# Optimization experiments

Measured on AMD Instinct MI355X. Metric: run time of the kernel, lower is better.

The kernel has to match this reference:

```python
import jax, jax.numpy as jnp
import numpy as np
import math

DIM = 1024

def setup_inputs() -> dict:
    key = jax.random.key(0)
    ks = jax.random.split(key, 5)
    X = jax.random.normal(ks[0], (4, 2048, DIM), dtype=jnp.float32)
    # Linear params (stored as [in, out] so y = x @ W + b)
    W_in = jax.random.normal(ks[1], (DIM, 3 * DIM), dtype=jnp.float32) / math.sqrt(DIM)
    b_in = jnp.zeros((3 * DIM,), dtype=jnp.float32)
    W_out = jax.random.normal(ks[2], (DIM, DIM), dtype=jnp.float32) / math.sqrt(DIM)
    b_out = jnp.zeros((DIM,), dtype=jnp.float32)
    return {"X": X, "W_in": W_in, "b_in": b_in, "W_out": W_out, "b_out": b_out}

def reference(X, W_in, b_in, W_out, b_out):
    dim = X.shape[-1]
    QKV = X @ W_in + b_in                       # [B, S, 3*dim]
    Q, K, V = jnp.split(QKV, 3, axis=-1)        # each [B, S, dim]
    scores = jnp.einsum('bqd,bkd->bqk', Q, K) / math.sqrt(dim)  # [B, S, S]
    attn = jax.nn.softmax(scores, axis=-1)
    out = jnp.einsum('bqk,bkd->bqd', attn, V)   # [B, S, dim]
    return out @ W_out + b_out
```

## Files before the change

### kernel.cpp

```cpp
#include <hip/hip_runtime.h>
#include <hip/hip_bf16.h>
#include <math.h>

typedef __attribute__((ext_vector_type(8))) __bf16 bf16x8;
typedef __attribute__((ext_vector_type(4))) float f32x4;
typedef __attribute__((ext_vector_type(4))) unsigned int u32x4;

#define DIM 1024
#define SEQ 2048
#define BATCH 4
#define ROWS (BATCH*SEQ)

#define BAR() do { asm volatile("" ::: "memory"); __builtin_amdgcn_s_barrier(); asm volatile("" ::: "memory"); } while(0)
#define WAITV(n) asm volatile("s_waitcnt vmcnt(" #n ")" ::: "memory")
#define WAITL0() asm volatile("s_waitcnt lgkmcnt(0)" ::: "memory")
#define SCHED0() __builtin_amdgcn_sched_barrier(0)
#define PRIO(x) __builtin_amdgcn_s_setprio(x)

#define DSR(d, a, off) do { u32x4 _t; \
  asm volatile("ds_read_b128 %0, %1 offset:" #off : "=v"(_t) : "v"(a)); \
  (d) = __builtin_bit_cast(bf16x8, _t); } while(0)

__device__ __forceinline__ unsigned short f2bf(float f) {
  unsigned int u = __float_as_uint(f);
  u += 0x7FFF + ((u >> 16) & 1);
  return (unsigned short)(u >> 16);
}
__device__ __forceinline__ unsigned short to_bf_bits(float v) { return f2bf(v); }
__device__ __forceinline__ unsigned short to_bf_bits(unsigned short v) { return v; }

__device__ __forceinline__ void gload_lds16(const void* g, void* lds) {
  __builtin_amdgcn_global_load_lds((__attribute__((address_space(1))) void*)g,
                                   (__attribute__((address_space(3))) void*)lds,
                                   16, 0, 0);
}

__global__ __launch_bounds__(256)
void conv_f32_bf16(const float* __restrict__ src, unsigned short* __restrict__ dst, int n8) {
  int i = blockIdx.x * blockDim.x + threadIdx.x;
  if (i >= n8) return;
  const float4* s = reinterpret_cast<const float4*>(src) + (size_t)i * 2;
  float4 a = s[0], b = s[1];
  union { unsigned short h[8]; uint4 v; } p;
  p.h[0]=f2bf(a.x); p.h[1]=f2bf(a.y); p.h[2]=f2bf(a.z); p.h[3]=f2bf(a.w);
  p.h[4]=f2bf(b.x); p.h[5]=f2bf(b.y); p.h[6]=f2bf(b.z); p.h[7]=f2bf(b.w);
  reinterpret_cast<uint4*>(dst)[i] = p.v;
}

template<typename Tin>
__global__ __launch_bounds__(1024)
void transpose_conv(const Tin* __restrict__ src, int ldsrc, size_t sstride,
                    unsigned short* __restrict__ dst, int lddst, size_t dstride) {
  __shared__ unsigned short tile[32][33];
  const Tin* s = src + (size_t)blockIdx.z * sstride;
  unsigned short* d = dst + (size_t)blockIdx.z * dstride;
  int tx = threadIdx.x, ty = threadIdx.y;
  int r = blockIdx.y * 32 + ty, c = blockIdx.x * 32 + tx;
  tile[ty][tx] = to_bf_bits(s[(size_t)r * ldsrc + c]);
  __syncthreads();
  d[(size_t)(blockIdx.x * 32 + ty) * lddst + blockIdx.y * 32 + tx] = tile[tx][ty];
}

#define EPI_QKV 0
#define EPI_F32 1
#define EPI_BF16 2
#define EPI_BIAS_F32 3

template<int BN, int EPI>
__global__ __launch_bounds__(512, 2)
void gemm8(const unsigned short* __restrict__ A, int lda, size_t sA,
           const unsigned short* __restrict__ B, int ldb, size_t sB,
           void* __restrict__ C, int ldc, size_t sC,
           const float* __restrict__ bias, int K) {
  constexpr int NREP = BN / 64;
  constexpr int NW = 16 * NREP;
  __shared__ unsigned short As[2 * 256 * 64];
  __shared__ unsigned short Bs[2 * BN * 64];

  const int tid = threadIdx.x;
  const int lane = tid & 63, wave = tid >> 6;
  const int wm = wave >> 2, wn = wave & 3;
  const int fr = lane & 15, fk = lane >> 4;
  const int tileM = blockIdx.y * 256, tileN = blockIdx.x * BN;
  const unsigned short* Ab = A + (size_t)blockIdx.z * sA;
  const unsigned short* Bb = B + (size_t)blockIdx.z * sB;

  const int srow = tid >> 3;
  const int sg = (tid & 7) ^ (srow & 7);

  auto stageA = [&](int buf, int half, int k0) {
#pragma unroll
    for (int q = 0; q < 2; ++q) {
      int rl = half * 128 + q * 64 + srow;
      gload_lds16(Ab + (size_t)(tileM + rl) * lda + k0 + sg * 8,
                  &As[buf * (256 * 64) + rl * 64 + (tid & 7) * 8]);
    }
  };
  auto stageB = [&](int buf, int half, int k0) {
#pragma unroll
    for (int q = 0; q < 2; ++q) {
      int rl = half * 128 + q * 64 + srow;
      gload_lds16(Bb + (size_t)(tileN + rl) * ldb + k0 + sg * 8,
                  &Bs[buf * (BN * 64) + rl * 64 + (tid & 7) * 8]);
    }
  };

  f32x4 acc[8][NREP];
#pragma unroll
  for (int m = 0; m < 8; ++m)
#pragma unroll
    for (int n = 0; n < NREP; ++n) acc[m][n] = (f32x4){0.f, 0.f, 0.f, 0.f};

  const int NS = K >> 6;
  const unsigned asb = (unsigned)(size_t)(__attribute__((address_space(3))) unsigned short*)As;
  const unsigned bsb = (unsigned)(size_t)(__attribute__((address_space(3))) unsigned short*)Bs;
  const unsigned aoff = (unsigned)((wm * 128 + fr) * 128 + ((fk ^ (fr & 7)) << 4));
  const unsigned boff = (unsigned)((wn * NW + fr) * 128 + ((fk ^ (fr & 7)) << 4));

  if constexpr (BN == 256) {
    stageB(0, 0, 0); stageB(0, 1, 0); stageA(0, 0, 0); stageA(0, 1, 0);
    if (NS > 1) { stageB(1, 0, 64); stageB(1, 1, 64); WAITV(4); } else { WAITV(0); }
  } else {
    stageB(0, 0, 0); stageA(0, 0, 0); stageA(0, 1, 0);
    if (NS > 1) { stageB(1, 0, 64); WAITV(2); } else { WAITV(0); }
  }
  BAR();

  bf16x8 afLo[4][2], afHi[4][2], bgA[2][2], bgB[2][2];

  for (int t = 0; t < NS; ++t) {
    const int cb = t & 1, nb = cb ^ 1;
    const unsigned aA0 = asb + (unsigned)cb * 32768u + aoff, aA1 = aA0 ^ 64u;
    const unsigned bB0 = bsb + (unsigned)cb * (unsigned)(BN * 128) + boff, bB1 = bB0 ^ 64u;
    const int k1 = (t + 1) << 6, k2 = (t + 2) << 6;

    if constexpr (BN == 256) {
      DSR(afLo[0][0], aA0, 0); DSR(afLo[1][0], aA0, 2048); DSR(afLo[2][0], aA0, 4096); DSR(afLo[3][0], aA0, 6144);
      DSR(afLo[0][1], aA1, 0); DSR(afLo[1][1], aA1, 2048); DSR(afLo[2][1], aA1, 4096); DSR(afLo[3][1], aA1, 6144);
      DSR(bgA[0][0], bB0, 0); DSR(bgA[1][0], bB0, 2048);
      DSR(bgA[0][1], bB1, 0); DSR(bgA[1][1], bB1, 2048);
      if (t + 1 < NS) stageA(nb, 0, k1);
      BAR(); WAITL0(); SCHED0();
      PRIO(1);
#pragma unroll
      for (int kk = 0; kk < 2; ++kk)
#pragma unroll
        for (int m = 0; m < 4; ++m)
#pragma unroll
          for (int n = 0; n < 2; ++n)
            acc[m][n] = __builtin_amdgcn_mfma_f32_16x16x32_bf16(afLo[m][kk], bgA[n][kk], acc[m][n], 0, 0, 0);
      PRIO(0); SCHED0();
      BAR();
      DSR(bgB[0][0], bB0, 4096); DSR(bgB[1][0], bB0, 6144);
      DSR(bgB[0][1], bB1, 4096); DSR(bgB[1][1], bB1, 6144);
      if (t + 1 < NS) stageA(nb, 1, k1);
      if (t + 2 < NS) stageB(cb, 0, k2);
      BAR(); WAITL0(); SCHED0();
      PRIO(1);
#pragma unroll
      for (int kk = 0; kk < 2; ++kk)
#pragma unroll
        for (int m = 0; m < 4; ++m)
#pragma unroll
          for (int n = 0; n < 2; ++n)
            acc[m][2 + n] = __builtin_amdgcn_mfma_f32_16x16x32_bf16(afLo[m][kk], bgB[n][kk], acc[m][2 + n], 0, 0, 0);
      PRIO(0); SCHED0();
      BAR();
      DSR(afHi[0][0], aA0, 8192); DSR(afHi[1][0], aA0, 10240); DSR(afHi[2][0], aA0, 12288); DSR(afHi[3][0], aA0, 14336);
      DSR(afHi[0][1], aA1, 8192); DSR(afHi[1][1], aA1, 10240); DSR(afHi[2][1], aA1, 12288); DSR(afHi[3][1], aA1, 14336);
      if (t + 2 < NS) stageB(cb, 1, k2);
      BAR(); WAITL0(); SCHED0();
      PRIO(1);
#pragma unroll
      for (int kk = 0; kk < 2; ++kk)
#pragma unroll
        for (int m = 0; m < 4; ++m)
#pragma unroll
          for (int n = 0; n < 2; ++n)
            acc[4 + m][n] = __builtin_amdgcn_mfma_f32_16x16x32_bf16(afHi[m][kk], bgA[n][kk], acc[4 + m][n], 0, 0, 0);
      PRIO(0); SCHED0();
      BAR();
      PRIO(1);
#pragma unroll
      for (int kk = 0; kk < 2; ++kk)
#pragma unroll
        for (int m = 0; m < 4; ++m)
#pragma unroll
          for (int n = 0; n < 2; ++n)
            acc[4 + m][2 + n] = __builtin_amdgcn_mfma_f32_16x16x32_bf16(afHi[m][kk], bgB[n][kk], acc[4 + m][2 + n], 0, 0, 0);
      PRIO(0); SCHED0();
      if (t + 1 < NS) { if (t + 2 < NS) { WAITV(4); } else { WAITV(0); } }
      BAR();
    } else {
      DSR(afLo[0][0], aA0, 0); DSR(afLo[1][0], aA0, 2048); DSR(afLo[2][0], aA0, 4096); DSR(afLo[3][0], aA0, 6144);
      DSR(bgA[0][0], bB0, 0); DSR(bgA[1][0], bB0, 2048);
      if (t + 1 < NS) stageA(nb, 0, k1);
      BAR(); WAITL0(); SCHED0();
      PRIO(1);
#pragma unroll
      for (int m = 0; m < 4; ++m)
#pragma unroll
        for (int n = 0; n < 2; ++n)
          acc[m][n] = __builtin_amdgcn_mfma_f32_16x16x32_bf16(afLo[m][0], bgA[n][0], acc[m][n], 0, 0, 0);
      PRIO(0); SCHED0();
      BAR();
      DSR(afLo[0][1], aA1, 0); DSR(afLo[1][1], aA1, 2048); DSR(afLo[2][1], aA1, 4096); DSR(afLo[3][1], aA1, 6144);
      DSR(bgA[0][1], bB1, 0); DSR(bgA[1][1], bB1, 2048);
      if (t + 1 < NS) stageA(nb, 1, k1);
      BAR(); WAITL0(); SCHED0();
      PRIO(1);
#pragma unroll
      for (int m = 0; m < 4; ++m)
#pragma unroll
        for (int n = 0; n < 2; ++n)
          acc[m][n] = __builtin_amdgcn_mfma_f32_16x16x32_bf16(afLo[m][1], bgA[n][1], acc[m][n], 0, 0, 0);
      PRIO(0); SCHED0();
      BAR();
      DSR(afHi[0][0], aA0, 8192); DSR(afHi[1][0], aA0, 10240); DSR(afHi[2][0], aA0, 12288); DSR(afHi[3][0], aA0, 14336);
      DSR(afHi[0][1], aA1, 8192); DSR(afHi[1][1], aA1, 10240); DSR(afHi[2][1], aA1, 12288); DSR(afHi[3][1], aA1, 14336);
      if (t + 2 < NS) stageB(cb, 0, k2);
      BAR(); WAITL0(); SCHED0();
      PRIO(1);
#pragma unroll
      for (int m = 0; m < 4; ++m)
#pragma unroll
        for (int n = 0; n < 2; ++n)
          acc[4 + m][n] = __builtin_amdgcn_mfma_f32_16x16x32_bf16(afHi[m][0], bgA[n][0], acc[4 + m][n], 0, 0, 0);
      PRIO(0); SCHED0();
      BAR();
      PRIO(1);
#pragma unroll
      for (int m = 0; m < 4; ++m)
#pragma unroll
        for (int n = 0; n < 2; ++n)
          acc[4 + m][n] = __builtin_amdgcn_mfma_f32_16x16x32_bf16(afHi[m][1], bgA[n][1], acc[4 + m][n], 0, 0, 0);
      PRIO(0); SCHED0();
      if (t + 1 < NS) { if (t + 2 < NS) { WAITV(2); } else { WAITV(0); } }
      BAR();
    }
  }

#pragma unroll
  for (int m = 0; m < 8; ++m)
#pragma unroll
    for (int n = 0; n < NREP; ++n)
#pragma unroll
      for (int j = 0; j < 4; ++j) {
        int row = tileM + wm * 128 + m * 16 + fk * 4 + j;
        int col = tileN + wn * NW + n * 16 + fr;
        float v = acc[m][n][j];
        if (EPI == EPI_QKV) {
          v += bias[col];
          if (col < DIM) v *= 0.03125f;
          ((unsigned short*)C + (size_t)blockIdx.z * sC)[(size_t)row * ldc + col] = f2bf(v);
        } else if (EPI == EPI_BF16) {
          ((unsigned short*)C + (size_t)blockIdx.z * sC)[(size_t)row * ldc + col] = f2bf(v);
        } else if (EPI == EPI_BIAS_F32) {
          ((float*)C + (size_t)blockIdx.z * sC)[(size_t)row * ldc + col] = v + bias[col];
        } else {
          ((float*)C + (size_t)blockIdx.z * sC)[(size_t)row * ldc + col] = v;
        }
      }
}

__global__ __launch_bounds__(256)
void softmax_kernel(float* __restrict__ S, size_t zstride) {
  __shared__ float red[8];
  float* row = S + (size_t)blockIdx.y * zstride + (size_t)blockIdx.x * SEQ;
  const int tid = threadIdx.x;
  const int lane = tid & 63, wave = tid >> 6;
  const float4* src = reinterpret_cast<const float4*>(row) + tid * 2;
  float4 a = src[0], b = src[1];
  float v[8] = {a.x, a.y, a.z, a.w, b.x, b.y, b.z, b.w};
  float m = v[0];
#pragma unroll
  for (int i = 1; i < 8; ++i) m = fmaxf(m, v[i]);
  for (int o = 32; o; o >>= 1) m = fmaxf(m, __shfl_xor(m, o));
  if (lane == 0) red[wave] = m;
  __syncthreads();
  m = fmaxf(fmaxf(red[0], red[1]), fmaxf(red[2], red[3]));
  float e[8], s = 0.f;
#pragma unroll
  for (int i = 0; i < 8; ++i) { e[i] = expf(v[i] - m); s += e[i]; }
  for (int o = 32; o; o >>= 1) s += __shfl_xor(s, o);
  if (lane == 0) red[4 + wave] = s;
  __syncthreads();
  s = red[4] + red[5] + red[6] + red[7];
  float inv = 1.f / s;
  union { unsigned short h[8]; uint4 u; } p;
#pragma unroll
  for (int i = 0; i < 8; ++i) p.h[i] = f2bf(e[i] * inv);
  reinterpret_cast<uint4*>(row)[tid] = p.u;
}

extern "C" void kernel_launch(void* const* d_in, const int* in_sizes, int n_in,
                              void* d_out, int out_size, void* d_ws, size_t ws_size,
                              hipStream_t stream) {
  const float* X     = (const float*)d_in[0];
  const float* W_in  = (const float*)d_in[1];
  const float* b_in  = (const float*)d_in[2];
  const float* W_out = (const float*)d_in[3];
  const float* b_out = (const float*)d_in[4];
  float* out = (float*)d_out;
  char* ws = (char*)d_ws;

  size_t o = 0;
  auto alloc = [&](size_t bytes) { size_t r = o; o += (bytes + 255) & ~(size_t)255; return r; };
  unsigned short* Xbf   = (unsigned short*)(ws + alloc((size_t)ROWS * DIM * 2));
  unsigned short* WinT  = (unsigned short*)(ws + alloc((size_t)3 * DIM * DIM * 2));
  unsigned short* WoutT = (unsigned short*)(ws + alloc((size_t)DIM * DIM * 2));
  unsigned short* QKV   = (unsigned short*)(ws + alloc((size_t)ROWS * 3 * DIM * 2));
  size_t fixed = o;
  size_t per_batch = (((size_t)SEQ * SEQ * 4 + 255) & ~(size_t)255) +
                     (((size_t)DIM * SEQ * 2 + 255) & ~(size_t)255);
  int G = (ws_size >= fixed + 4 * per_batch) ? BATCH : 1;
  float*          Sc = (float*)(ws + alloc((size_t)G * SEQ * SEQ * 4));
  unsigned short* Vt = (unsigned short*)(ws + alloc((size_t)G * DIM * SEQ * 2));
  unsigned short* O  = Xbf;

  conv_f32_bf16<<<(ROWS * DIM / 8 + 255) / 256, 256, 0, stream>>>(X, Xbf, ROWS * DIM / 8);
  transpose_conv<float><<<dim3(3 * DIM / 32, DIM / 32, 1), dim3(32, 32), 0, stream>>>(
      W_in, 3 * DIM, 0, WinT, DIM, 0);
  transpose_conv<float><<<dim3(DIM / 32, DIM / 32, 1), dim3(32, 32), 0, stream>>>(
      W_out, DIM, 0, WoutT, DIM, 0);
  gemm8<256, EPI_QKV><<<dim3(3 * DIM / 256, ROWS / 256, 1), 512, 0, stream>>>(
      Xbf, DIM, 0, WinT, DIM, 0, QKV, 3 * DIM, 0, b_in, DIM);

  for (int b0 = 0; b0 < BATCH; b0 += G) {
    const unsigned short* Qb = QKV + (size_t)b0 * SEQ * 3 * DIM;
    const unsigned short* Kb = Qb + DIM;
    const unsigned short* Vb = Qb + 2 * DIM;
    transpose_conv<unsigned short><<<dim3(DIM / 32, SEQ / 32, G), dim3(32, 32), 0, stream>>>(
        Vb, 3 * DIM, (size_t)SEQ * 3 * DIM, Vt, SEQ, (size_t)DIM * SEQ);
    gemm8<256, EPI_F32><<<dim3(SEQ / 256, SEQ / 256, G), 512, 0, stream>>>(
        Qb, 3 * DIM, (size_t)SEQ * 3 * DIM, Kb, 3 * DIM, (size_t)SEQ * 3 * DIM,
        Sc, SEQ, (size_t)SEQ * SEQ, nullptr, DIM);
    softmax_kernel<<<dim3(SEQ, G), 256, 0, stream>>>(Sc, (size_t)SEQ * SEQ);
    gemm8<128, EPI_BF16><<<dim3(DIM / 128, SEQ / 256, G), 512, 0, stream>>>(
        (const unsigned short*)Sc, 2 * SEQ, (size_t)2 * SEQ * SEQ,
        Vt, SEQ, (size_t)DIM * SEQ,
        O + (size_t)b0 * SEQ * DIM, DIM, (size_t)SEQ * DIM, nullptr, SEQ);
  }
  gemm8<128, EPI_BIAS_F32><<<dim3(DIM / 128, ROWS / 256, 1), 512, 0, stream>>>(
      O, DIM, 0, WoutT, DIM, 0, out, DIM, 0, b_out, DIM);
}
```

Before: 229.5 us.

## Software-pipeline LDS fragment reads across MFMA phases and use BN=128 for QKV GEMM

Restructures both GEMM variants so LDS fragment loads for the next phase, and for the next k-tile, are issued before the current MFMA block. Full lgkmcnt(0) waits become partial waits, letting ds_reads overlap with matrix math. The QKV projection also switches from the 256-wide to the 128-wide tile config, doubling grid size. The cost is higher register pressure from extra fragment buffers and a more fragile wait-count schedule.

```diff
diff --git a/kernel.cpp b/kernel.cpp
--- a/kernel.cpp
+++ b/kernel.cpp
@@ -13,7 +13,7 @@
 
 #define BAR() do { asm volatile("" ::: "memory"); __builtin_amdgcn_s_barrier(); asm volatile("" ::: "memory"); } while(0)
 #define WAITV(n) asm volatile("s_waitcnt vmcnt(" #n ")" ::: "memory")
-#define WAITL0() asm volatile("s_waitcnt lgkmcnt(0)" ::: "memory")
+#define WAITL(n) asm volatile("s_waitcnt lgkmcnt(" #n ")" ::: "memory")
 #define SCHED0() __builtin_amdgcn_sched_barrier(0)
 #define PRIO(x) __builtin_amdgcn_s_setprio(x)
 
@@ -116,126 +116,151 @@
   const unsigned bsb = (unsigned)(size_t)(__attribute__((address_space(3))) unsigned short*)Bs;
   const unsigned aoff = (unsigned)((wm * 128 + fr) * 128 + ((fk ^ (fr & 7)) << 4));
   const unsigned boff = (unsigned)((wn * NW + fr) * 128 + ((fk ^ (fr & 7)) << 4));
+  auto aBase = [&](int b) { return asb + (unsigned)b * 32768u + aoff; };
+  auto bBase = [&](int b) { return bsb + (unsigned)b * (unsigned)(BN * 128) + boff; };
 
   if constexpr (BN == 256) {
+    bf16x8 afLo[4][2], afHi[4][2], bgA[2][2], bgB[2][2];
     stageB(0, 0, 0); stageB(0, 1, 0); stageA(0, 0, 0); stageA(0, 1, 0);
     if (NS > 1) { stageB(1, 0, 64); stageB(1, 1, 64); WAITV(4); } else { WAITV(0); }
+    BAR();
+    {
+      unsigned a0 = aBase(0), a1 = a0 ^ 64u, b0 = bBase(0), b1 = b0 ^ 64u;
+      DSR(afLo[0][0], a0, 0); DSR(afLo[1][0], a0, 2048); DSR(afLo[2][0], a0, 4096); DSR(afLo[3][0], a0, 6144);
+      DSR(afLo[0][1], a1, 0); DSR(afLo[1][1], a1, 2048); DSR(afLo[2][1], a1, 4096); DSR(afLo[3][1], a1, 6144);
+      DSR(bgA[0][0], b0, 0); DSR(bgA[1][0], b0, 2048);
+      DSR(bgA[0][1], b1, 0); DSR(bgA[1][1], b1, 2048);
+    }
+    for (int t = 0; t < NS; ++t) {
+      const int cb = t & 1, nb = cb ^ 1;
+      const unsigned cA0 = aBase(cb), cA1 = cA0 ^ 64u, cB0 = bBase(cb), cB1 = cB0 ^ 64u;
+      const unsigned nA0 = aBase(nb), nA1 = nA0 ^ 64u, nB0 = bBase(nb), nB1 = nB0 ^ 64u;
+      const int k1 = (t + 1) << 6, k2 = (t + 2) << 6;
+      DSR(bgB[0][0], cB0, 4096); DSR(bgB[1][0], cB0, 6144);
+      DSR(bgB[0][1], cB1, 4096); DSR(bgB[1][1], cB1, 6144);
+      if (t + 1 < NS) stageA(nb, 0, k1);
+      BAR(); WAITL(4); SCHED0();
+      PRIO(1);
+#pragma unroll
+      for (int kk = 0; kk < 2; ++kk)
+#pragma unroll
+        for (int m = 0; m < 4; ++m)
+#pragma unroll
+          for (int n = 0; n < 2; ++n)
+            acc[m][n] = __builtin_amdgcn_mfma_f32_16x16x32_bf16(afLo[m][kk], bgA[n][kk], acc[m][n], 0, 0, 0);
+      PRIO(0); SCHED0();
+      BAR();
+      DSR(afHi[0][0], cA0, 8192); DSR(afHi[1][0], cA0, 10240); DSR(afHi[2][0], cA0, 12288); DSR(afHi[3][0], cA0, 14336);
+      DSR(afHi[0][1], cA1, 8192); DSR(afHi[1][1], cA1, 10240); DSR(afHi[2][1], cA1, 12288); DSR(afHi[3][1], cA1, 14336);
+      if (t + 1 < NS) stageA(nb, 1, k1);
+      if (t + 2 < NS) stageB(cb, 0, k2);
+      BAR(); WAITL(8); SCHED0();
+      PRIO(1);
+#pragma unroll
+      for (int kk = 0; kk < 2; ++kk)
+#pragma unroll
+        for (int m = 0; m < 4; ++m)
+#pragma unroll
+          for (int n = 0; n < 2; ++n)
+            acc[m][2 + n] = __builtin_amdgcn_mfma_f32_16x16x32_bf16(afLo[m][kk], bgB[n][kk], acc[m][2 + n], 0, 0, 0);
+      PRIO(0); SCHED0();
+      BAR();
+      if (t + 2 < NS) stageB(cb, 1, k2);
+      BAR(); WAITL(0); SCHED0();
+      PRIO(1);
+#pragma unroll
+      for (int kk = 0; kk < 2; ++kk)
+#pragma unroll
+        for (int m = 0; m < 4; ++m)
+#pragma unroll
+          for (int n = 0; n < 2; ++n)
+            acc[4 + m][n] = __builtin_amdgcn_mfma_f32_16x16x32_bf16(afHi[m][kk], bgA[n][kk], acc[4 + m][n], 0, 0, 0);
+      PRIO(0); SCHED0();
+      if (t + 1 < NS) { if (t + 2 < NS) { WAITV(4); } else { WAITV(0); } }
+      BAR();
+      if (t + 1 < NS) {
+        DSR(afLo[0][0], nA0, 0); DSR(afLo[1][0], nA0, 2048); DSR(afLo[2][0], nA0, 4096); DSR(afLo[3][0], nA0, 6144);
+        DSR(afLo[0][1], nA1, 0); DSR(afLo[1][1], nA1, 2048); DSR(afLo[2][1], nA1, 4096); DSR(afLo[3][1], nA1, 6144);
+        DSR(bgA[0][0], nB0, 0); DSR(bgA[1][0], nB0, 2048);
+        DSR(bgA[0][1], nB1, 0); DSR(bgA[1][1], nB1, 2048);
+      }
+      SCHED0();
+      PRIO(1);
+#pragma unroll
+      for (int kk = 0; kk < 2; ++kk)
+#pragma unroll
+        for (int m = 0; m < 4; ++m)
+#pragma unroll
+          for (int n = 0; n < 2; ++n)
+            acc[4 + m][2 + n] = __builtin_amdgcn_mfma_f32_16x16x32_bf16(afHi[m][kk], bgB[n][kk], acc[4 + m][2 + n], 0, 0, 0);
+      PRIO(0); SCHED0();
+      BAR();
+    }
   } else {
+    bf16x8 a0f[4], a1f[4], h0f[4], h1f[4], b0f[2], b1f[2];
     stageB(0, 0, 0); stageA(0, 0, 0); stageA(0, 1, 0);
     if (NS > 1) { stageB(1, 0, 64); WAITV(2); } else { WAITV(0); }
-  }
-  BAR();
-
-  bf16x8 afLo[4][2], afHi[4][2], bgA[2][2], bgB[2][2];
-
-  for (int t = 0; t < NS; ++t) {
-    const int cb = t & 1, nb = cb ^ 1;
-    const unsigned aA0 = asb + (unsigned)cb * 32768u + aoff, aA1 = aA0 ^ 64u;
-    const unsigned bB0 = bsb + (unsigned)cb * (unsigned)(BN * 128) + boff, bB1 = bB0 ^ 64u;
-    const int k1 = (t + 1) << 6, k2 = (t + 2) << 6;
-
-    if constexpr (BN == 256) {
-      DSR(afLo[0][0], aA0, 0); DSR(afLo[1][0], aA0, 2048); DSR(afLo[2][0], aA0, 4096); DSR(afLo[3][0], aA0, 6144);
-      DSR(afLo[0][1], aA1, 0); DSR(afLo[1][1], aA1, 2048); DSR(afLo[2][1], aA1, 4096); DSR(afLo[3][1], aA1, 6144);
-      DSR(bgA[0][0], bB0, 0); DSR(bgA[1][0], bB0, 2048);
-      DSR(bgA[0][1], bB1, 0); DSR(bgA[1][1], bB1, 2048);
+    BAR();
+    {
+      unsigned a0 = aBase(0), b0 = bBase(0);
+      DSR(a0f[0], a0, 0); DSR(a0f[1], a0, 2048); DSR(a0f[2], a0, 4096); DSR(a0f[3], a0, 6144);
+      DSR(b0f[0], b0, 0); DSR(b0f[1], b0, 2048);
+    }
+    for (int t = 0; t < NS; ++t) {
+      const int cb = t & 1, nb = cb ^ 1;
+      const unsigned cA0 = aBase(cb), cA1 = cA0 ^ 64u, cB0 = bBase(cb), cB1 = cB0 ^ 64u;
+      const unsigned nA0 = aBase(nb), nB0 = bBase(nb);
+      const int k1 = (t + 1) << 6, k2 = (t + 2) << 6;
+      DSR(a1f[0], cA1, 0); DSR(a1f[1], cA1, 2048); DSR(a1f[2], cA1, 4096); DSR(a1f[3], cA1, 6144);
+      DSR(b1f[0], cB1, 0); DSR(b1f[1], cB1, 2048);
       if (t + 1 < NS) stageA(nb, 0, k1);
-      BAR(); WAITL0(); SCHED0();
-      PRIO(1);
-#pragma unroll
-      for (int kk = 0; kk < 2; ++kk)
-#pragma unroll
-        for (int m = 0; m < 4; ++m)
-#pragma unroll
-          for (int n = 0; n < 2; ++n)
-            acc[m][n] = __builtin_amdgcn_mfma_f32_16x16x32_bf16(afLo[m][kk], bgA[n][kk], acc[m][n], 0, 0, 0);
-      PRIO(0); SCHED0();
-      BAR();
-      DSR(bgB[0][0], bB0, 4096); DSR(bgB[1][0], bB0, 6144);
-      DSR(bgB[0][1], bB1, 4096); DSR(bgB[1][1], bB1, 6144);
+      BAR(); WAITL(6); SCHED0();
+      PRIO(1);
+#pragma unroll
+      for (int m = 0; m < 4; ++m)
+#pragma unroll
+        for (int n = 0; n < 2; ++n)
+          acc[m][n] = __builtin_amdgcn_mfma_f32_16x16x32_bf16(a0f[m], b0f[n], acc[m][n], 0, 0, 0);
+      PRIO(0); SCHED0();
+      BAR();
+      DSR(h0f[0], cA0, 8192); DSR(h0f[1], cA0, 10240); DSR(h0f[2], cA0, 12288); DSR(h0f[3], cA0, 14336);
       if (t + 1 < NS) stageA(nb, 1, k1);
+      BAR(); WAITL(4); SCHED0();
+      PRIO(1);
+#pragma unroll
+      for (int m = 0; m < 4; ++m)
+#pragma unroll
+        for (int n = 0; n < 2; ++n)
+          acc[m][n] = __builtin_amdgcn_mfma_f32_16x16x32_bf16(a1f[m], b1f[n], acc[m][n], 0, 0, 0);
+      PRIO(0); SCHED0();
+      BAR();
+      DSR(h1f[0], cA1, 8192); DSR(h1f[1], cA1, 10240); DSR(h1f[2], cA1, 12288); DSR(h1f[3], cA1, 14336);
       if (t + 2 < NS) stageB(cb, 0, k2);
-      BAR(); WAITL0(); SCHED0();
-      PRIO(1);
-#pragma unroll
-      for (int kk = 0; kk < 2; ++kk)
-#pragma unroll
-        for (int m = 0; m < 4; ++m)
-#pragma unroll
-          for (int n = 0; n < 2; ++n)
-            acc[m][2 + n] = __builtin_amdgcn_mfma_f32_16x16x32_bf16(afLo[m][kk], bgB[n][kk], acc[m][2 + n], 0, 0, 0);
-      PRIO(0); SCHED0();
-      BAR();
-      DSR(afHi[0][0], aA0, 8192); DSR(afHi[1][0], aA0, 10240); DSR(afHi[2][0], aA0, 12288); DSR(afHi[3][0], aA0, 14336);
-      DSR(afHi[0][1], aA1, 8192); DSR(afHi[1][1], aA1, 10240); DSR(afHi[2][1], aA1, 12288); DSR(afHi[3][1], aA1, 14336);
-      if (t + 2 < NS) stageB(cb, 1, k2);
-      BAR(); WAITL0(); SCHED0();
-      PRIO(1);
-#pragma unroll
-      for (int kk = 0; kk < 2; ++kk)
-#pragma unroll
-        for (int m = 0; m < 4; ++m)
-#pragma unroll
-          for (int n = 0; n < 2; ++n)
-            acc[4 + m][n] = __builtin_amdgcn_mfma_f32_16x16x32_bf16(afHi[m][kk], bgA[n][kk], acc[4 + m][n], 0, 0, 0);
-      PRIO(0); SCHED0();
-      BAR();
-      PRIO(1);
-#pragma unroll
-      for (int kk = 0; kk < 2; ++kk)
-#pragma unroll
-        for (int m = 0; m < 4; ++m)
-#pragma unroll
-          for (int n = 0; n < 2; ++n)
-            acc[4 + m][2 + n] = __builtin_amdgcn_mfma_f32_16x16x32_bf16(afHi[m][kk], bgB[n][kk], acc[4 + m][2 + n], 0, 0, 0);
-      PRIO(0); SCHED0();
-      if (t + 1 < NS) { if (t + 2 < NS) { WAITV(4); } else { WAITV(0); } }
-      BAR();
-    } else {
-      DSR(afLo[0][0], aA0, 0); DSR(afLo[1][0], aA0, 2048); DSR(afLo[2][0], aA0, 4096); DSR(afLo[3][0], aA0, 6144);
-      DSR(bgA[0][0], bB0, 0); DSR(bgA[1][0], bB0, 2048);
-      if (t + 1 < NS) stageA(nb, 0, k1);
-      BAR(); WAITL0(); SCHED0();
+      BAR(); WAITL(4); SCHED0();
       PRIO(1);
 #pragma unroll
       for (int m = 0; m < 4; ++m)
 #pragma unroll
         for (int n = 0; n < 2; ++n)
-          acc[m][n] = __builtin_amdgcn_mfma_f32_16x16x32_bf16(afLo[m][0], bgA[n][0], acc[m][n], 0, 0, 0);
-      PRIO(0); SCHED0();
-      BAR();
-      DSR(afLo[0][1], aA1, 0); DSR(afLo[1][1], aA1, 2048); DSR(afLo[2][1], aA1, 4096); DSR(afLo[3][1], aA1, 6144);
-      DSR(bgA[0][1], bB1, 0); DSR(bgA[1][1], bB1, 2048);
-      if (t + 1 < NS) stageA(nb, 1, k1);
-      BAR(); WAITL0(); SCHED0();
+          acc[4 + m][n] = __builtin_amdgcn_mfma_f32_16x16x32_bf16(h0f[m], b0f[n], acc[4 + m][n], 0, 0, 0);
+      PRIO(0); SCHED0();
+      if (t + 1 < NS) { if (t + 2 < NS) { WAITV(2); } else { WAITV(0); } }
+      BAR();
+      if (t + 1 < NS) {
+        DSR(a0f[0], nA0, 0); DSR(a0f[1], nA0, 2048); DSR(a0f[2], nA0, 4096); DSR(a0f[3], nA0, 6144);
+        DSR(b0f[0], nB0, 0); DSR(b0f[1], nB0, 2048);
+        WAITL(6);
+      } else {
+        WAITL(0);
+      }
+      SCHED0();
       PRIO(1);
 #pragma unroll
       for (int m = 0; m < 4; ++m)
 #pragma unroll
         for (int n = 0; n < 2; ++n)
-          acc[m][n] = __builtin_amdgcn_mfma_f32_16x16x32_bf16(afLo[m][1], bgA[n][1], acc[m][n], 0, 0, 0);
-      PRIO(0); SCHED0();
-      BAR();
-      DSR(afHi[0][0], aA0, 8192); DSR(afHi[1][0], aA0, 10240); DSR(afHi[2][0], aA0, 12288); DSR(afHi[3][0], aA0, 14336);
-      DSR(afHi[0][1], aA1, 8192); DSR(afHi[1][1], aA1, 10240); DSR(afHi[2][1], aA1, 12288); DSR(afHi[3][1], aA1, 14336);
-      if (t + 2 < NS) stageB(cb, 0, k2);
-      BAR(); WAITL0(); SCHED0();
-      PRIO(1);
-#pragma unroll
-      for (int m = 0; m < 4; ++m)
-#pragma unroll
-        for (int n = 0; n < 2; ++n)
-          acc[4 + m][n] = __builtin_amdgcn_mfma_f32_16x16x32_bf16(afHi[m][0], bgA[n][0], acc[4 + m][n], 0, 0, 0);
-      PRIO(0); SCHED0();
-      BAR();
-      PRIO(1);
-#pragma unroll
-      for (int m = 0; m < 4; ++m)
-#pragma unroll
-        for (int n = 0; n < 2; ++n)
-          acc[4 + m][n] = __builtin_amdgcn_mfma_f32_16x16x32_bf16(afHi[m][1], bgA[n][1], acc[4 + m][n], 0, 0, 0);
-      PRIO(0); SCHED0();
-      if (t + 1 < NS) { if (t + 2 < NS) { WAITV(2); } else { WAITV(0); } }
+          acc[4 + m][n] = __builtin_amdgcn_mfma_f32_16x16x32_bf16(h1f[m], b1f[n], acc[4 + m][n], 0, 0, 0);
+      PRIO(0); SCHED0();
       BAR();
     }
   }
@@ -323,7 +348,7 @@
       W_in, 3 * DIM, 0, WinT, DIM, 0);
   transpose_conv<float><<<dim3(DIM / 32, DIM / 32, 1), dim3(32, 32), 0, stream>>>(
       W_out, DIM, 0, WoutT, DIM, 0);
-  gemm8<256, EPI_QKV><<<dim3(3 * DIM / 256, ROWS / 256, 1), 512, 0, stream>>>(
+  gemm8<128, EPI_QKV><<<dim3(3 * DIM / 128, ROWS / 256, 1), 512, 0, stream>>>(
       Xbf, DIM, 0, WinT, DIM, 0, QKV, 3 * DIM, 0, b_in, DIM);
 
   for (int b0 = 0; b0 < BATCH; b0 += G) {
```

New measurement: 228.5 us. About the same (-0.4%).
